# Optimization experiments

Hardware: AMD Instinct MI355X
Metric: run time of the kernel (lower is better)

## Reference

```python
import jax, jax.numpy as jnp
import numpy as np

TEMPERATURE = 0.1
EPS_NORM = 1e-12  # torch F.normalize eps
EPS_LOSS = 1e-8


def setup_inputs() -> dict:
    key = jax.random.key(0)
    k1, k2 = jax.random.split(key)
    N, D, K = 8192, 512, 64
    features = jax.random.normal(k1, (N, D), dtype=jnp.float32)
    cluster_assignments = jax.random.randint(k2, (N,), 0, K, dtype=jnp.int64)
    return {"features": features, "cluster_assignments": cluster_assignments}


def reference(features, cluster_assignments):
    # L2 normalize rows (torch.nn.functional.normalize, p=2, dim=1)
    norm = jnp.linalg.norm(features, axis=1, keepdims=True)
    features_norm = features / jnp.maximum(norm, EPS_NORM)
    # pairwise cosine similarity scaled by temperature -> [N, N]
    sim = jnp.einsum('id,jd->ij', features_norm, features_norm) / TEMPERATURE
    exp_sim = jnp.exp(sim)
    mask = (cluster_assignments[None, :] == cluster_assignments[:, None]).astype(exp_sim.dtype)
    pos_sum = jnp.sum(exp_sim * mask, axis=1, keepdims=True)
    neg_sum = jnp.sum(exp_sim * (1.0 - mask), axis=1, keepdims=True)
    loss = -jnp.log(pos_sum / (pos_sum + neg_sum + EPS_LOSS))
    return jnp.sum(loss)  # reduction='sum'
```

## Files before the change

### kernel.cpp

```cpp
#include <hip/hip_runtime.h>
#include <hip/hip_bf16.h>
#include <stdint.h>

#define N 8192
#define D 512
#define TILE 128
#define BK 64
#define NKC (D / BK)
#define NTB (N / TILE)
#define NBLK (NTB * (NTB + 1) / 2)
#define PANEL_BYTES (TILE * D)
#define KCHUNK_BYTES (TILE * BK)

typedef long long i64;
typedef __attribute__((ext_vector_type(4))) float f32x4;

__device__ __forceinline__ void gload_lds16(const void* gp, const void* lp) {
    auto g = (const __attribute__((address_space(1))) void*)(uintptr_t)gp;
    auto l = (__attribute__((address_space(3))) void*)(uintptr_t)lp;
    __builtin_amdgcn_global_load_lds(g, l, 16, 0, 0);
}

__global__ void cc_normalize(const float* __restrict__ F, uint8_t* __restrict__ Fn2,
                             float* __restrict__ out) {
    if (blockIdx.x == 0 && threadIdx.x == 0) out[0] = 0.0f;
    const int row  = blockIdx.x * 4 + (threadIdx.x >> 6);
    const int lane = threadIdx.x & 63;
    const float* p = F + (size_t)row * D + lane * 8;
    float4 a = *(const float4*)p;
    float4 b = *(const float4*)(p + 4);
    float ss = a.x*a.x + a.y*a.y + a.z*a.z + a.w*a.w
             + b.x*b.x + b.y*b.y + b.z*b.z + b.w*b.w;
    #pragma unroll
    for (int m = 32; m; m >>= 1) ss += __shfl_xor(ss, m, 64);
    const float inv = 16.0f / fmaxf(sqrtf(ss), 1e-12f);
    int lo = 0, hi = 0;
    lo = __builtin_amdgcn_cvt_pk_fp8_f32(a.x*inv, a.y*inv, lo, false);
    lo = __builtin_amdgcn_cvt_pk_fp8_f32(a.z*inv, a.w*inv, lo, true);
    hi = __builtin_amdgcn_cvt_pk_fp8_f32(b.x*inv, b.y*inv, hi, false);
    hi = __builtin_amdgcn_cvt_pk_fp8_f32(b.z*inv, b.w*inv, hi, true);
    const size_t idx = (size_t)(row >> 7) * PANEL_BYTES + (size_t)lane * 1024 + (row & 127) * 8;
    *(int2*)(Fn2 + idx) = make_int2(lo, hi);
}

__global__ __launch_bounds__(256, 3)
void cc_gemm(const uint8_t* __restrict__ Fn2, const int* __restrict__ cl,
             float* __restrict__ Pt, float* __restrict__ Pp) {
    __shared__ __align__(16) uint8_t smem[6 * KCHUNK_BYTES];
    __shared__ int crow[TILE], ccol[TILE];
    uint8_t* As = smem;
    uint8_t* Bs = smem + 3 * KCHUNK_BYTES;
    float (*rsum)[TILE][2] = (float (*)[TILE][2])(smem);
    float (*csum)[TILE][2] = (float (*)[TILE][2])(smem + 4096);

    const int tid  = threadIdx.x;
    const int wave = tid >> 6;
    const int lane = tid & 63;

    int rem = blockIdx.x, bm = 0;
    while (rem >= NTB - bm) { rem -= NTB - bm; ++bm; }
    const int bn = bm + rem;
    const bool diag = (bm == bn);

    if (tid < TILE)            crow[tid]        = cl[bm * TILE + tid];
    else                       ccol[tid - TILE] = cl[bn * TILE + (tid - TILE)];

    const int wr = wave >> 1, wc = wave & 1;
    const int q   = lane >> 4;
    const int n15 = lane & 15;

    f32x4 acc[4][4];
    #pragma unroll
    for (int t = 0; t < 4; ++t)
        #pragma unroll
        for (int u = 0; u < 4; ++u) acc[t][u] = (f32x4)(0.0f);

    const uint8_t* Ag = Fn2 + (size_t)bm * PANEL_BYTES;
    const uint8_t* Bg = Fn2 + (size_t)bn * PANEL_BYTES;

    auto stage = [&](int kc, int buf) {
        const uint8_t* ga = Ag + kc * KCHUNK_BYTES;
        const uint8_t* gb = Bg + kc * KCHUNK_BYTES;
        #pragma unroll
        for (int i = 0; i < 2; ++i) {
            const int off = (wave * 2 + i) * 1024;
            gload_lds16(ga + off + lane * 16, As + buf * KCHUNK_BYTES + off);
            gload_lds16(gb + off + lane * 16, Bs + buf * KCHUNK_BYTES + off);
        }
    };

    stage(0, 0);
    stage(1, 1);

    #pragma unroll
    for (int kc = 0; kc < NKC; ++kc) {
        const int b = kc % 3;
        if (kc < NKC - 1)
            asm volatile("s_waitcnt vmcnt(4) lgkmcnt(0)\n\ts_barrier" ::: "memory");
        else
            asm volatile("s_waitcnt vmcnt(0) lgkmcnt(0)\n\ts_barrier" ::: "memory");
        if (kc + 2 < NKC) stage(kc + 2, (kc + 2) % 3);
        #pragma unroll
        for (int ks = 0; ks < 2; ++ks) {
            const int base = b * KCHUNK_BYTES + ks * 4096 + q * 1024 + n15 * 8;
            i64 af[4], bfr[4];
            #pragma unroll
            for (int t = 0; t < 4; ++t)
                af[t] = *(const i64*)&As[base + (wr * 64 + t * 16) * 8];
            #pragma unroll
            for (int u = 0; u < 4; ++u)
                bfr[u] = *(const i64*)&Bs[base + (wc * 64 + u * 16) * 8];
            #pragma unroll
            for (int t = 0; t < 4; ++t)
                #pragma unroll
                for (int u = 0; u < 4; ++u)
                    acc[t][u] = __builtin_amdgcn_mfma_f32_16x16x32_fp8_fp8(af[t], bfr[u], acc[t][u], 0, 0, 0);
        }
    }

    __syncthreads();

    const float SC = 0.05635527503472514f;
    int cc[4];
    #pragma unroll
    for (int u = 0; u < 4; ++u) cc[u] = ccol[wc * 64 + u * 16 + n15];

    float ce[4] = {0.f, 0.f, 0.f, 0.f};
    float cp[4] = {0.f, 0.f, 0.f, 0.f};

    #pragma unroll
    for (int t = 0; t < 4; ++t) {
        #pragma unroll
        for (int r = 0; r < 4; ++r) {
            const int lr  = wr * 64 + t * 16 + q * 4 + r;
            const int myc = crow[lr];
            float te = 0.0f, tp = 0.0f;
            #pragma unroll
            for (int u = 0; u < 4; ++u) {
                const float e  = exp2f(acc[t][u][r] * SC);
                const float ep = (cc[u] == myc) ? e : 0.0f;
                te += e;  tp += ep;
                ce[u] += e;  cp[u] += ep;
            }
            #pragma unroll
            for (int m = 1; m < 16; m <<= 1) {
                te += __shfl_xor(te, m, 64);
                tp += __shfl_xor(tp, m, 64);
            }
            if (n15 == 0) { rsum[wc][lr][0] = te; rsum[wc][lr][1] = tp; }
        }
    }

    if (!diag) {
        #pragma unroll
        for (int u = 0; u < 4; ++u) {
            float e = ce[u], p2 = cp[u];
            e += __shfl_xor(e, 16, 64);  p2 += __shfl_xor(p2, 16, 64);
            e += __shfl_xor(e, 32, 64);  p2 += __shfl_xor(p2, 32, 64);
            if (lane < 16) {
                const int lc = wc * 64 + u * 16 + n15;
                csum[wr][lc][0] = e;  csum[wr][lc][1] = p2;
            }
        }
    }

    __syncthreads();
    if (tid < TILE) {
        const float te = rsum[0][tid][0] + rsum[1][tid][0];
        const float tp = rsum[0][tid][1] + rsum[1][tid][1];
        const size_t o = (size_t)bn * N + bm * TILE + tid;
        Pt[o] = te;  Pp[o] = tp;
    } else if (!diag) {
        const int c = tid - TILE;
        const float te = csum[0][c][0] + csum[1][c][0];
        const float tp = csum[0][c][1] + csum[1][c][1];
        const size_t o = (size_t)bm * N + bn * TILE + c;
        Pt[o] = te;  Pp[o] = tp;
    }
}

__global__ void cc_finalize(const float* __restrict__ Pt, const float* __restrict__ Pp,
                            float* __restrict__ out) {
    __shared__ float red[4];
    const int i = blockIdx.x * 256 + threadIdx.x;
    float tv = 0.0f, pv = 0.0f;
    #pragma unroll 8
    for (int s = 0; s < NTB; ++s) {
        tv += Pt[(size_t)s * N + i];
        pv += Pp[(size_t)s * N + i];
    }
    float l = __logf(tv + 1e-8f) - __logf(pv);
    #pragma unroll
    for (int m = 32; m; m >>= 1) l += __shfl_xor(l, m, 64);
    const int wv = threadIdx.x >> 6, lane = threadIdx.x & 63;
    if (lane == 0) red[wv] = l;
    __syncthreads();
    if (threadIdx.x == 0) atomicAdd(out, red[0] + red[1] + red[2] + red[3]);
}

extern "C" void kernel_launch(void* const* d_in, const int* in_sizes, int n_in,
                              void* d_out, int out_size, void* d_ws, size_t ws_size,
                              hipStream_t stream) {
    const float* F  = (const float*)d_in[0];
    const int*   cl = (const int*)d_in[1];
    float* out = (float*)d_out;

    uint8_t* Fn2 = (uint8_t*)d_ws;
    float* Pt  = (float*)((char*)d_ws + (size_t)N * D);
    float* Pp  = Pt + (size_t)NTB * N;

    cc_normalize<<<N / 4, 256, 0, stream>>>(F, Fn2, out);
    cc_gemm<<<NBLK, 256, 0, stream>>>(Fn2, cl, Pt, Pp);
    cc_finalize<<<N / 256, 256, 0, stream>>>(Pt, Pp, out);
}
```

Measured before the change: 125.0 us.

## Fuse normalize, GEMM and finalize into one cooperative persistent kernel

Replaces the three kernel launches with a single cooperative kernel of 512 persistent blocks. Grid-wide syncs separate the normalize, tiled GEMM and finalize phases, and the GEMM tiles are distributed in a grid-stride loop. The row and column partial-sum reductions are rewritten as transpose-style butterfly shuffles, so each lane ends up owning one row's sum and the shuffle count drops. This aims to remove launch gaps and reduction overhead, at the cost of grid sync latency, uneven tile distribution (2080 tiles over 512 blocks) and a lower occupancy bound.

```diff
diff --git a/kernel.cpp b/kernel.cpp
--- a/kernel.cpp
+++ b/kernel.cpp
@@ -1,4 +1,5 @@
 #include <hip/hip_runtime.h>
+#include <hip/hip_cooperative_groups.h>
 #include <hip/hip_bf16.h>
 #include <stdint.h>
 
@@ -9,11 +10,14 @@
 #define NKC (D / BK)
 #define NTB (N / TILE)
 #define NBLK (NTB * (NTB + 1) / 2)
+#define GRID2 512
 #define PANEL_BYTES (TILE * D)
 #define KCHUNK_BYTES (TILE * BK)
 
 typedef long long i64;
 typedef __attribute__((ext_vector_type(4))) float f32x4;
+
+namespace cg = cooperative_groups;
 
 __device__ __forceinline__ void gload_lds16(const void* gp, const void* lp) {
     auto g = (const __attribute__((address_space(1))) void*)(uintptr_t)gp;
@@ -21,11 +25,9 @@
     __builtin_amdgcn_global_load_lds(g, l, 16, 0, 0);
 }
 
-__global__ void cc_normalize(const float* __restrict__ F, uint8_t* __restrict__ Fn2,
-                             float* __restrict__ out) {
-    if (blockIdx.x == 0 && threadIdx.x == 0) out[0] = 0.0f;
-    const int row  = blockIdx.x * 4 + (threadIdx.x >> 6);
-    const int lane = threadIdx.x & 63;
+__device__ __forceinline__ void normalize_row(const float* __restrict__ F,
+                                              uint8_t* __restrict__ Fn2,
+                                              int row, int lane) {
     const float* p = F + (size_t)row * D + lane * 8;
     float4 a = *(const float4*)p;
     float4 b = *(const float4*)(p + 4);
@@ -43,21 +45,18 @@
     *(int2*)(Fn2 + idx) = make_int2(lo, hi);
 }
 
-__global__ __launch_bounds__(256, 3)
-void cc_gemm(const uint8_t* __restrict__ Fn2, const int* __restrict__ cl,
-             float* __restrict__ Pt, float* __restrict__ Pp) {
+__device__ __forceinline__ void gemm_tile(int bi, const uint8_t* __restrict__ Fn2,
+                                          const int* __restrict__ cl,
+                                          float* __restrict__ Pt, float* __restrict__ Pp,
+                                          int tid, int wave, int lane) {
     __shared__ __align__(16) uint8_t smem[6 * KCHUNK_BYTES];
     __shared__ int crow[TILE], ccol[TILE];
     uint8_t* As = smem;
     uint8_t* Bs = smem + 3 * KCHUNK_BYTES;
-    float (*rsum)[TILE][2] = (float (*)[TILE][2])(smem);
-    float (*csum)[TILE][2] = (float (*)[TILE][2])(smem + 4096);
-
-    const int tid  = threadIdx.x;
-    const int wave = tid >> 6;
-    const int lane = tid & 63;
-
-    int rem = blockIdx.x, bm = 0;
+    float2 (*rsum)[TILE] = (float2 (*)[TILE])(smem);
+    float2 (*csum)[TILE] = (float2 (*)[TILE])(smem + 4096);
+
+    int rem = bi, bm = 0;
     while (rem >= NTB - bm) { rem -= NTB - bm; ++bm; }
     const int bn = bm + rem;
     const bool diag = (bm == bn);
@@ -88,6 +87,8 @@
             gload_lds16(gb + off + lane * 16, Bs + buf * KCHUNK_BYTES + off);
         }
     };
+
+    __syncthreads();
 
     stage(0, 0);
     stage(1, 1);
@@ -125,64 +126,90 @@
     #pragma unroll
     for (int u = 0; u < 4; ++u) cc[u] = ccol[wc * 64 + u * 16 + n15];
 
+    float ra[16], rp[16];
     float ce[4] = {0.f, 0.f, 0.f, 0.f};
-    float cp[4] = {0.f, 0.f, 0.f, 0.f};
+    float cp2[4] = {0.f, 0.f, 0.f, 0.f};
 
     #pragma unroll
     for (int t = 0; t < 4; ++t) {
         #pragma unroll
         for (int r = 0; r < 4; ++r) {
-            const int lr  = wr * 64 + t * 16 + q * 4 + r;
-            const int myc = crow[lr];
+            const int myc = crow[wr * 64 + t * 16 + q * 4 + r];
             float te = 0.0f, tp = 0.0f;
             #pragma unroll
             for (int u = 0; u < 4; ++u) {
                 const float e  = exp2f(acc[t][u][r] * SC);
                 const float ep = (cc[u] == myc) ? e : 0.0f;
                 te += e;  tp += ep;
-                ce[u] += e;  cp[u] += ep;
+                ce[u] += e;  cp2[u] += ep;
             }
-            #pragma unroll
-            for (int m = 1; m < 16; m <<= 1) {
-                te += __shfl_xor(te, m, 64);
-                tp += __shfl_xor(tp, m, 64);
+            ra[t * 4 + r] = te;  rp[t * 4 + r] = tp;
+        }
+    }
+
+    {
+        int len = 16;
+        #pragma unroll
+        for (int m = 1; m <= 8; m <<= 1) {
+            const int half = len >> 1;
+            const bool hiL = (lane & m) != 0;
+            #pragma unroll
+            for (int j = 0; j < half; ++j) {
+                float sa = hiL ? ra[j] : ra[j + half];
+                float sp = hiL ? rp[j] : rp[j + half];
+                sa = __shfl_xor(sa, m, 64);
+                sp = __shfl_xor(sp, m, 64);
+                ra[j] = (hiL ? ra[j + half] : ra[j]) + sa;
+                rp[j] = (hiL ? rp[j + half] : rp[j]) + sp;
             }
-            if (n15 == 0) { rsum[wc][lr][0] = te; rsum[wc][lr][1] = tp; }
-        }
+            len = half;
+        }
+        const int idx = ((n15 & 1) << 3) | ((n15 & 2) << 1) | ((n15 & 4) >> 1) | ((n15 & 8) >> 3);
+        const int row = wr * 64 + (idx >> 2) * 16 + q * 4 + (idx & 3);
+        rsum[wc][row] = make_float2(ra[0], rp[0]);
     }
 
     if (!diag) {
-        #pragma unroll
-        for (int u = 0; u < 4; ++u) {
-            float e = ce[u], p2 = cp[u];
-            e += __shfl_xor(e, 16, 64);  p2 += __shfl_xor(p2, 16, 64);
-            e += __shfl_xor(e, 32, 64);  p2 += __shfl_xor(p2, 32, 64);
-            if (lane < 16) {
-                const int lc = wc * 64 + u * 16 + n15;
-                csum[wr][lc][0] = e;  csum[wr][lc][1] = p2;
+        int len = 4;
+        #pragma unroll
+        for (int m = 16; m <= 32; m <<= 1) {
+            const int half = len >> 1;
+            const bool hiL = (lane & m) != 0;
+            #pragma unroll
+            for (int j = 0; j < half; ++j) {
+                float se = hiL ? ce[j] : ce[j + half];
+                float sp = hiL ? cp2[j] : cp2[j + half];
+                se = __shfl_xor(se, m, 64);
+                sp = __shfl_xor(sp, m, 64);
+                ce[j] = (hiL ? ce[j + half] : ce[j]) + se;
+                cp2[j] = (hiL ? cp2[j + half] : cp2[j]) + sp;
             }
-        }
+            len = half;
+        }
+        const int u = (((lane >> 4) & 1) << 1) | ((lane >> 5) & 1);
+        const int col = wc * 64 + u * 16 + n15;
+        csum[wr][col] = make_float2(ce[0], cp2[0]);
     }
 
     __syncthreads();
     if (tid < TILE) {
-        const float te = rsum[0][tid][0] + rsum[1][tid][0];
-        const float tp = rsum[0][tid][1] + rsum[1][tid][1];
+        const float2 r0 = rsum[0][tid], r1 = rsum[1][tid];
         const size_t o = (size_t)bn * N + bm * TILE + tid;
-        Pt[o] = te;  Pp[o] = tp;
+        Pt[o] = r0.x + r1.x;  Pp[o] = r0.y + r1.y;
     } else if (!diag) {
         const int c = tid - TILE;
-        const float te = csum[0][c][0] + csum[1][c][0];
-        const float tp = csum[0][c][1] + csum[1][c][1];
+        const float2 c0 = csum[0][c], c1 = csum[1][c];
         const size_t o = (size_t)bm * N + bn * TILE + c;
-        Pt[o] = te;  Pp[o] = tp;
-    }
-}
-
-__global__ void cc_finalize(const float* __restrict__ Pt, const float* __restrict__ Pp,
-                            float* __restrict__ out) {
+        Pt[o] = c0.x + c1.x;  Pp[o] = c0.y + c1.y;
+    }
+}
+
+__device__ __forceinline__ void finalize_chunk(const float* __restrict__ Pt,
+                                               const float* __restrict__ Pp,
+                                               float* __restrict__ out,
+                                               int blk, int tid, int wave, int lane) {
     __shared__ float red[4];
-    const int i = blockIdx.x * 256 + threadIdx.x;
+    const int i = blk * 256 + tid;
     float tv = 0.0f, pv = 0.0f;
     #pragma unroll 8
     for (int s = 0; s < NTB; ++s) {
@@ -192,10 +219,50 @@
     float l = __logf(tv + 1e-8f) - __logf(pv);
     #pragma unroll
     for (int m = 32; m; m >>= 1) l += __shfl_xor(l, m, 64);
-    const int wv = threadIdx.x >> 6, lane = threadIdx.x & 63;
-    if (lane == 0) red[wv] = l;
-    __syncthreads();
-    if (threadIdx.x == 0) atomicAdd(out, red[0] + red[1] + red[2] + red[3]);
+    if (lane == 0) red[wave] = l;
+    __syncthreads();
+    if (tid == 0) atomicAdd(out, red[0] + red[1] + red[2] + red[3]);
+}
+
+__global__ void cc_normalize(const float* __restrict__ F, uint8_t* __restrict__ Fn2,
+                             float* __restrict__ out) {
+    if (blockIdx.x == 0 && threadIdx.x == 0) out[0] = 0.0f;
+    normalize_row(F, Fn2, blockIdx.x * 4 + (threadIdx.x >> 6), threadIdx.x & 63);
+}
+
+__global__ __launch_bounds__(256, 3)
+void cc_gemm(const uint8_t* __restrict__ Fn2, const int* __restrict__ cl,
+             float* __restrict__ Pt, float* __restrict__ Pp) {
+    gemm_tile(blockIdx.x, Fn2, cl, Pt, Pp, threadIdx.x, threadIdx.x >> 6, threadIdx.x & 63);
+}
+
+__global__ void cc_finalize(const float* __restrict__ Pt, const float* __restrict__ Pp,
+                            float* __restrict__ out) {
+    finalize_chunk(Pt, Pp, out, blockIdx.x, threadIdx.x, threadIdx.x >> 6, threadIdx.x & 63);
+}
+
+__global__ __launch_bounds__(256, 2)
+void cc_all(const float* __restrict__ F, const int* __restrict__ cl,
+            uint8_t* __restrict__ Fn2, float* __restrict__ Pt,
+            float* __restrict__ Pp, float* __restrict__ out) {
+    const int tid  = threadIdx.x;
+    const int wave = tid >> 6;
+    const int lane = tid & 63;
+
+    {
+        const int wid = blockIdx.x * 4 + wave;
+        #pragma unroll
+        for (int r = 0; r < 4; ++r) normalize_row(F, Fn2, wid * 4 + r, lane);
+        if (blockIdx.x == 0 && tid == 0) out[0] = 0.0f;
+    }
+    cg::this_grid().sync();
+
+    for (int bi = blockIdx.x; bi < NBLK; bi += GRID2)
+        gemm_tile(bi, Fn2, cl, Pt, Pp, tid, wave, lane);
+
+    cg::this_grid().sync();
+
+    if (blockIdx.x < 32) finalize_chunk(Pt, Pp, out, blockIdx.x, tid, wave, lane);
 }
 
 extern "C" void kernel_launch(void* const* d_in, const int* in_sizes, int n_in,
@@ -209,7 +276,13 @@
     float* Pt  = (float*)((char*)d_ws + (size_t)N * D);
     float* Pp  = Pt + (size_t)NTB * N;
 
-    cc_normalize<<<N / 4, 256, 0, stream>>>(F, Fn2, out);
-    cc_gemm<<<NBLK, 256, 0, stream>>>(Fn2, cl, Pt, Pp);
-    cc_finalize<<<N / 256, 256, 0, stream>>>(Pt, Pp, out);
-}
+    void* args[] = { (void*)&F, (void*)&cl, (void*)&Fn2, (void*)&Pt, (void*)&Pp, (void*)&out };
+    hipError_t e = hipLaunchCooperativeKernel((const void*)cc_all, dim3(GRID2), dim3(256),
+                                              args, 0, stream);
+    if (e != hipSuccess) {
+        (void)hipGetLastError();
+        cc_normalize<<<N / 4, 256, 0, stream>>>(F, Fn2, out);
+        cc_gemm<<<NBLK, 256, 0, stream>>>(Fn2, cl, Pt, Pp);
+        cc_finalize<<<N / 256, 256, 0, stream>>>(Pt, Pp, out);
+    }
+}
```

Result: slower. 246.3 us (+97.1%).
